# Performance work log

Hardware: AMD Instinct MI355X
Metric: run time of the kernel (lower is better)

The kernel has to match this reference:

```python
import jax, jax.numpy as jnp
import numpy as np

N_POS = 1024
N_NEG = 5
D = 128
N_LEM = 20000
MOMENTUM = 0.5
EPS = 1e-12

def _l2norm(m):
    n = jnp.sqrt(jnp.sum(m * m, axis=1, keepdims=True))
    return m / jnp.maximum(n, EPS)

def setup_inputs() -> dict:
    key = jax.random.key(0)
    k1, k2, k3, k4 = jax.random.split(key, 4)
    B = 8
    x = jax.random.normal(k1, (B, N_POS + N_NEG, D), dtype=jnp.float32)
    y = jax.random.randint(k2, (B, N_POS), 0, N_POS, dtype=jnp.int64)
    visible = jax.random.randint(k3, (B, N_POS), 0, 2, dtype=jnp.int32)
    stdv = 1.0 / np.sqrt(D / 3)
    memory = jax.random.uniform(k4, (N_LEM, D), dtype=jnp.float32,
                                minval=-stdv, maxval=stdv)
    return {"x": x, "y": y, "visible": visible, "memory": memory, "lru": 0}

def reference(x, y, visible, memory, lru):
    B = x.shape[0]
    x_pos = x[:, :N_POS, :]            # [B, n_pos, D]
    x_neg = x[:, N_POS:, :]            # [B, n_neg, D]

    # similarity of positives against full memory bank: [B, n_pos, nLem]
    similarity = jnp.einsum('bpd,md->bpm', x_pos, memory)
    # noise similarity against first n_pos memory rows: [B, n_neg, n_pos]
    noise_similarity = jnp.einsum('bnd,md->bnm', x_neg, memory[:N_POS])

    y_idx = y.astype(jnp.int64)  # group_size == 1

    # scatter-accumulate: one-hot(y)^T @ (x_pos * visible), mean over batch
    vals = (x_pos * visible.astype(x.dtype)[..., None]).reshape(-1, D)
    ids = y.reshape(-1)
    get = jax.ops.segment_sum(vals, ids, num_segments=N_POS) / B  # [n_pos, D]

    # momentum EMA on positive rows + LRU insertion of noise features
    mem_pos = memory[:N_POS] * MOMENTUM + get * (1.0 - MOMENTUM)
    start = N_POS + lru * N_NEG * B   # lru is a python int -> static slice
    neg_parts = jnp.concatenate([
        memory[N_POS:start],
        x_neg.reshape(-1, D),
        memory[start + N_NEG * B:],
    ], axis=0)
    new_memory = _l2norm(jnp.concatenate([mem_pos, neg_parts], axis=0))

    return similarity, y_idx, noise_similarity, new_memory
```

## Files before the change

### kernel.cpp

```cpp
#include <hip/hip_runtime.h>
#include <stdint.h>

#define NPOS 1024
#define NNEG 5
#define DD   128
#define NLEM 20000
#define BB   8
#define NTOK 1029

#define OFF_Y     163840000ULL
#define OFF_NOISE 163848192ULL
#define OFF_NM    163889152ULL

typedef short bf16x8 __attribute__((ext_vector_type(8)));
typedef float f32x4  __attribute__((ext_vector_type(4)));

__device__ __forceinline__ uint16_t f2bf(float f) {
  union { float f; uint32_t u; } c; c.f = f;
  uint32_t u = c.u;
  return (uint16_t)((u + 0x7FFFu + ((u >> 16) & 1u)) >> 16);
}

__global__ void convert_x(const float* __restrict__ x, uint16_t* __restrict__ xb) {
  int t = blockIdx.x * 256 + threadIdx.x;
  int e = t * 4;
  int row = e >> 7;
  int d   = e & 127;
  int b = row >> 10, p = row & 1023;
  float4 v = *(const float4*)(x + ((size_t)(b * NTOK + p)) * DD + d);
  ushort4 o;
  o.x = f2bf(v.x); o.y = f2bf(v.y); o.z = f2bf(v.z); o.w = f2bf(v.w);
  *(ushort4*)(xb + e) = o;
}

__global__ void convert_mem(const float* __restrict__ m, uint16_t* __restrict__ mb) {
  size_t e = ((size_t)blockIdx.x * 256 + threadIdx.x) * 4;
  float4 v = *(const float4*)(m + e);
  ushort4 o;
  o.x = f2bf(v.x); o.y = f2bf(v.y); o.z = f2bf(v.z); o.w = f2bf(v.w);
  *(ushort4*)(mb + e) = o;
}

__global__ __launch_bounds__(256) void sim_mfma(const uint16_t* __restrict__ Xb,
                                                const uint16_t* __restrict__ Mb,
                                                float* __restrict__ out) {
  const int lane = threadIdx.x & 63;
  const int wave = threadIdx.x >> 6;
  const int wr = wave >> 1;
  const int wc = wave & 1;
  const int row0 = blockIdx.y * 128 + wr * 64;
  const int col0 = blockIdx.x * 160 + wc * 80;
  const int lrow = lane & 15;
  const int kk0  = (lane >> 4) * 8;

  f32x4 acc[4][5] = {};

  const uint16_t* xp = Xb + (size_t)(row0 + lrow) * DD + kk0;
  const uint16_t* mp = Mb + (size_t)(col0 + lrow) * DD + kk0;

  #pragma unroll
  for (int k0 = 0; k0 < DD; k0 += 32) {
    bf16x8 a[4], b[5];
    #pragma unroll
    for (int i = 0; i < 4; i++) a[i] = *(const bf16x8*)(xp + (size_t)(16 * i) * DD + k0);
    #pragma unroll
    for (int j = 0; j < 5; j++) b[j] = *(const bf16x8*)(mp + (size_t)(16 * j) * DD + k0);
    #pragma unroll
    for (int i = 0; i < 4; i++)
      #pragma unroll
      for (int j = 0; j < 5; j++)
        acc[i][j] = __builtin_amdgcn_mfma_f32_16x16x32_bf16(a[i], b[j], acc[i][j], 0, 0, 0);
  }

  const int rb = (lane >> 4) * 4;
  const int cb = lane & 15;
  #pragma unroll
  for (int i = 0; i < 4; i++) {
    #pragma unroll
    for (int j = 0; j < 5; j++) {
      size_t base = (size_t)(row0 + 16 * i + rb) * NLEM + (size_t)(col0 + 16 * j + cb);
      #pragma unroll
      for (int t = 0; t < 4; t++)
        out[base + (size_t)t * NLEM] = acc[i][j][t];
    }
  }
}

__global__ void sim_f32(const float* __restrict__ x, const float* __restrict__ mem,
                        float* __restrict__ out) {
  size_t idx = (size_t)blockIdx.x * 256 + threadIdx.x;
  if (idx >= (size_t)BB * NPOS * NLEM) return;
  int col = (int)(idx % NLEM);
  int row = (int)(idx / NLEM);
  int b = row >> 10, p = row & 1023;
  const float* xr = x + ((size_t)(b * NTOK + p)) * DD;
  const float* mr = mem + (size_t)col * DD;
  float s = 0.f;
  #pragma unroll 8
  for (int d = 0; d < DD; d += 4) {
    float4 xv = *(const float4*)(xr + d);
    float4 mv = *(const float4*)(mr + d);
    s = fmaf(xv.x, mv.x, s); s = fmaf(xv.y, mv.y, s);
    s = fmaf(xv.z, mv.z, s); s = fmaf(xv.w, mv.w, s);
  }
  out[idx] = s;
}

__global__ void noise_sim(const float* __restrict__ x, const float* __restrict__ mem,
                          float* __restrict__ on) {
  int t = blockIdx.x * 256 + threadIdx.x;
  int m = t & (NPOS - 1);
  int r = t >> 10;
  int b = r / NNEG, n = r - b * NNEG;
  const float* xr = x + ((size_t)(b * NTOK) + NPOS + n) * DD;
  const float* mr = mem + (size_t)m * DD;
  float s = 0.f;
  #pragma unroll 8
  for (int d = 0; d < DD; d += 4) {
    float4 xv = *(const float4*)(xr + d);
    float4 mv = *(const float4*)(mr + d);
    s = fmaf(xv.x, mv.x, s); s = fmaf(xv.y, mv.y, s);
    s = fmaf(xv.z, mv.z, s); s = fmaf(xv.w, mv.w, s);
  }
  on[t] = s;
}

__global__ void ycopy(const int* __restrict__ y, float* __restrict__ oy) {
  int t = blockIdx.x * 256 + threadIdx.x;
  oy[t] = (float)y[t];
}

__global__ void scatter_seg(const float* __restrict__ x, const int* __restrict__ y,
                            const int* __restrict__ visible, float* acc) {
  int t = blockIdx.x * 256 + threadIdx.x;
  int row = t >> 7;
  int d   = t & 127;
  if (visible[row]) {
    int b = row >> 10, p = row & 1023;
    float v = x[((size_t)(b * NTOK + p)) * DD + d];
    atomicAdd(&acc[(size_t)y[row] * DD + d], v);
  }
}

__global__ void newmem_kernel(const float* __restrict__ mem, const float* __restrict__ x,
                              const int* __restrict__ lru, float* nm) {
  int row  = blockIdx.x * 4 + (threadIdx.x >> 6);
  int lane = threadIdx.x & 63;
  int start = NPOS + lru[0] * NNEG * BB;
  int d = lane * 2;
  float2 v;
  if (row < NPOS) {
    float2 mv = *(const float2*)(mem + (size_t)row * DD + d);
    float2 av = *(const float2*)(nm + (size_t)row * DD + d);
    v.x = 0.5f * mv.x + 0.0625f * av.x;
    v.y = 0.5f * mv.y + 0.0625f * av.y;
  } else if (row >= start && row < start + NNEG * BB) {
    int r = row - start;
    int b = r / NNEG, n = r - b * NNEG;
    v = *(const float2*)(x + ((size_t)(b * NTOK) + NPOS + n) * DD + d);
  } else {
    v = *(const float2*)(mem + (size_t)row * DD + d);
  }
  float ss = v.x * v.x + v.y * v.y;
  #pragma unroll
  for (int off = 1; off < 64; off <<= 1) ss += __shfl_xor(ss, off, 64);
  float inv = 1.0f / fmaxf(sqrtf(ss), 1e-12f);
  float2 o; o.x = v.x * inv; o.y = v.y * inv;
  *(float2*)(nm + (size_t)row * DD + d) = o;
}

extern "C" void kernel_launch(void* const* d_in, const int* in_sizes, int n_in,
                              void* d_out, int out_size, void* d_ws, size_t ws_size,
                              hipStream_t stream) {
  const float* x       = (const float*)d_in[0];
  const int*   y       = (const int*)d_in[1];
  const int*   visible = (const int*)d_in[2];
  const float* memory  = (const float*)d_in[3];
  const int*   lru     = (const int*)d_in[4];
  float* out = (float*)d_out;

  float* out_sim   = out;
  float* out_y     = out + OFF_Y;
  float* out_noise = out + OFF_NOISE;
  float* out_nm    = out + OFF_NM;

  hipMemsetAsync(out_nm, 0, (size_t)NPOS * DD * sizeof(float), stream);

  size_t need = (size_t)BB * NPOS * DD * 2 + (size_t)NLEM * DD * 2;
  if (ws_size >= need) {
    uint16_t* xb = (uint16_t*)d_ws;
    uint16_t* mb = xb + (size_t)BB * NPOS * DD;
    convert_x<<<1024, 256, 0, stream>>>(x, xb);
    convert_mem<<<2500, 256, 0, stream>>>(memory, mb);
    dim3 g(125, 64);
    sim_mfma<<<g, 256, 0, stream>>>(xb, mb, out_sim);
  } else {
    sim_f32<<<640000, 256, 0, stream>>>(x, memory, out_sim);
  }
  noise_sim<<<160, 256, 0, stream>>>(x, memory, out_noise);
  ycopy<<<32, 256, 0, stream>>>(y, out_y);
  scatter_seg<<<4096, 256, 0, stream>>>(x, y, visible, out_nm);
  newmem_kernel<<<5000, 256, 0, stream>>>(memory, x, lru, out_nm);
}
```

Before: 779.5 us.

## Stage GEMM operand tiles in padded LDS and shrink row tile to 64

The similarity MFMA kernel now loads a 64x128 X tile and a 160x128 memory tile cooperatively into shared memory, padding rows to avoid bank conflicts. Waves then read MFMA fragments from LDS instead of issuing strided global loads per lane. The block row tile drops from 128 to 64, which doubles the grid and cuts accumulators per wave. The kernel is dominated by writing the large fp32 output, so operand-load changes may matter little, and the smaller tile re-reads the memory bank twice as often.

```diff
diff --git a/kernel.cpp b/kernel.cpp
--- a/kernel.cpp
+++ b/kernel.cpp
@@ -14,6 +14,8 @@
 
 typedef short bf16x8 __attribute__((ext_vector_type(8)));
 typedef float f32x4  __attribute__((ext_vector_type(4)));
+
+#define LDS_STRIDE 136
 
 __device__ __forceinline__ uint16_t f2bf(float f) {
   union { float f; uint32_t u; } c; c.f = f;
@@ -44,29 +46,48 @@
 __global__ __launch_bounds__(256) void sim_mfma(const uint16_t* __restrict__ Xb,
                                                 const uint16_t* __restrict__ Mb,
                                                 float* __restrict__ out) {
-  const int lane = threadIdx.x & 63;
-  const int wave = threadIdx.x >> 6;
+  __shared__ uint16_t Xs[64 * LDS_STRIDE];
+  __shared__ uint16_t Ms[160 * LDS_STRIDE];
+
+  const int tid  = threadIdx.x;
+  const int lane = tid & 63;
+  const int wave = tid >> 6;
   const int wr = wave >> 1;
   const int wc = wave & 1;
-  const int row0 = blockIdx.y * 128 + wr * 64;
-  const int col0 = blockIdx.x * 160 + wc * 80;
+  const int row0 = blockIdx.y * 64;
+  const int col0 = blockIdx.x * 160;
+
+  #pragma unroll
+  for (int it = 0; it < 4; it++) {
+    int c = it * 256 + tid;
+    int r = c >> 4, cc = c & 15;
+    bf16x8 v = *(const bf16x8*)(Xb + (size_t)(row0 + r) * DD + cc * 8);
+    *(bf16x8*)(Xs + r * LDS_STRIDE + cc * 8) = v;
+  }
+  #pragma unroll
+  for (int it = 0; it < 10; it++) {
+    int c = it * 256 + tid;
+    int r = c >> 4, cc = c & 15;
+    bf16x8 v = *(const bf16x8*)(Mb + (size_t)(col0 + r) * DD + cc * 8);
+    *(bf16x8*)(Ms + r * LDS_STRIDE + cc * 8) = v;
+  }
+  __syncthreads();
+
   const int lrow = lane & 15;
   const int kk0  = (lane >> 4) * 8;
-
-  f32x4 acc[4][5] = {};
-
-  const uint16_t* xp = Xb + (size_t)(row0 + lrow) * DD + kk0;
-  const uint16_t* mp = Mb + (size_t)(col0 + lrow) * DD + kk0;
+  f32x4 acc[2][5] = {};
 
   #pragma unroll
   for (int k0 = 0; k0 < DD; k0 += 32) {
-    bf16x8 a[4], b[5];
-    #pragma unroll
-    for (int i = 0; i < 4; i++) a[i] = *(const bf16x8*)(xp + (size_t)(16 * i) * DD + k0);
-    #pragma unroll
-    for (int j = 0; j < 5; j++) b[j] = *(const bf16x8*)(mp + (size_t)(16 * j) * DD + k0);
-    #pragma unroll
-    for (int i = 0; i < 4; i++)
+    bf16x8 a[2], b[5];
+    #pragma unroll
+    for (int i = 0; i < 2; i++)
+      a[i] = *(const bf16x8*)(Xs + (32 * wr + 16 * i + lrow) * LDS_STRIDE + k0 + kk0);
+    #pragma unroll
+    for (int j = 0; j < 5; j++)
+      b[j] = *(const bf16x8*)(Ms + (80 * wc + 16 * j + lrow) * LDS_STRIDE + k0 + kk0);
+    #pragma unroll
+    for (int i = 0; i < 2; i++)
       #pragma unroll
       for (int j = 0; j < 5; j++)
         acc[i][j] = __builtin_amdgcn_mfma_f32_16x16x32_bf16(a[i], b[j], acc[i][j], 0, 0, 0);
@@ -75,10 +96,11 @@
   const int rb = (lane >> 4) * 4;
   const int cb = lane & 15;
   #pragma unroll
-  for (int i = 0; i < 4; i++) {
+  for (int i = 0; i < 2; i++) {
     #pragma unroll
     for (int j = 0; j < 5; j++) {
-      size_t base = (size_t)(row0 + 16 * i + rb) * NLEM + (size_t)(col0 + 16 * j + cb);
+      size_t base = (size_t)(row0 + 32 * wr + 16 * i + rb) * NLEM
+                  + (size_t)(col0 + 80 * wc + 16 * j + cb);
       #pragma unroll
       for (int t = 0; t < 4; t++)
         out[base + (size_t)t * NLEM] = acc[i][j][t];
@@ -192,7 +214,7 @@
     uint16_t* mb = xb + (size_t)BB * NPOS * DD;
     convert_x<<<1024, 256, 0, stream>>>(x, xb);
     convert_mem<<<2500, 256, 0, stream>>>(memory, mb);
-    dim3 g(125, 64);
+    dim3 g(125, 128);
     sim_mfma<<<g, 256, 0, stream>>>(xb, mb, out_sim);
   } else {
     sim_f32<<<640000, 256, 0, stream>>>(x, memory, out_sim);
```

Result: faster. 757.4 us (-2.8%).
